# Performance work log

Hardware: AMD Instinct MI355X
Metric: run time of the kernel (lower is better)

The kernel has to match this reference:

```python
import jax, jax.numpy as jnp
import numpy as np
from jax import lax

H, P, N, G, K, CHUNK = 64, 64, 128, 1, 4, 256
D_MODEL = 2048
D_INNER = H * P            # 4096
CONV_DIM = D_INNER + 2 * G * N  # 4352
EPS = 1e-5


def setup_inputs() -> dict:
    key = jax.random.key(0)
    ks = jax.random.split(key, 6)
    s = lambda k, shape, scale: jax.random.normal(k, shape, jnp.float32) * scale
    return {
        "hidden_states": s(ks[0], (2, 2048, D_MODEL), 1.0),
        "in_proj_w": s(ks[1], (D_MODEL, D_INNER + CONV_DIM + H), D_MODEL ** -0.5),
        "conv_w": s(ks[2], (CONV_DIM, K), K ** -0.5),
        "conv_b": jnp.zeros((CONV_DIM,), jnp.float32),
        "dt_bias": jnp.ones((H,), jnp.float32),
        "A_log": jnp.log(jnp.arange(1, H + 1, dtype=jnp.float32)),
        "D_param": jnp.ones((H,), jnp.float32),
        "norm_w": jnp.ones((D_INNER,), jnp.float32),
        "out_proj_w": s(ks[3], (D_INNER, D_MODEL), D_INNER ** -0.5),
    }


def _mamba2_forward(hidden_states, in_proj_w, conv_w, conv_b, dt_bias, A_log, D_param, norm_w, out_proj_w):
    b, l, _ = hidden_states.shape
    c = l // CHUNK  # number of chunks

    # in_proj -> gate | conv channels (x,B,C) | dt
    proj = hidden_states @ in_proj_w
    gate = proj[..., :D_INNER]
    hbc = proj[..., D_INNER:D_INNER + CONV_DIM]
    dt = proj[..., D_INNER + CONV_DIM:]  # [b,l,H]

    # depthwise causal conv1d + silu
    xt = hbc.transpose(0, 2, 1)  # [b, CONV_DIM, l]
    y = lax.conv_general_dilated(
        xt, conv_w[:, None, :], window_strides=(1,), padding=[(K - 1, 0)],
        feature_group_count=CONV_DIM, dimension_numbers=("NCH", "OIH", "NCH"))
    hbc = jax.nn.silu(y + conv_b[None, :, None]).transpose(0, 2, 1)  # [b,l,CONV_DIM]

    # split into x / B / C per group (unflatten over groups as in torch code)
    per_g = D_INNER // G
    hg = hbc.reshape(b, l, G, per_g + 2 * N)
    x = hg[..., :per_g].reshape(b, l, H, P)                 # [b,l,h,p]
    Bm = hg[..., per_g:per_g + N]                            # [b,l,g,n]
    Cm = hg[..., per_g + N:]                                 # [b,l,g,n]
    hpg = H // G
    Bh = jnp.repeat(Bm, hpg, axis=2)                         # [b,l,h,n]
    Ch = jnp.repeat(Cm, hpg, axis=2)

    # dt: softplus(dt + bias), clamp per time_step_limit (0, inf)
    dt = jax.nn.softplus(dt + dt_bias)                       # [b,l,h]
    A = -jnp.exp(A_log)                                      # [h]

    # chunk the sequence
    x_c = x.reshape(b, c, CHUNK, H, P)
    B_c = Bh.reshape(b, c, CHUNK, H, N)
    C_c = Ch.reshape(b, c, CHUNK, H, N)
    dt_c = dt.reshape(b, c, CHUNK, H)

    dA = dt_c * A[None, None, None, :]                       # [b,c,L,h]
    cum = jnp.cumsum(dA, axis=2)                             # [b,c,L,h]

    # intra-chunk (diagonal block): decay[i,j] = exp(cum_i - cum_j), i>=j
    diff = cum[:, :, :, None, :] - cum[:, :, None, :, :]     # [b,c,i,j,h]
    i = jnp.arange(CHUNK)
    mask = i[:, None] >= i[None, :]
    decay = jnp.exp(jnp.where(mask[None, None, :, :, None], diff, -jnp.inf))
    scores = jnp.einsum("bcihn,bcjhn->bcijh", C_c, B_c) * decay * dt_c[:, :, None, :, :]
    Y_diag = jnp.einsum("bcijh,bcjhp->bcihp", scores, x_c)   # [b,c,L,h,p]

    # per-chunk final states
    decay_states = jnp.exp(cum[:, :, -1:, :] - cum)          # [b,c,L,h]
    states = jnp.einsum("bclh,bclhn,bclhp->bchpn", decay_states * dt_c, B_c, x_c)
    chunk_decay = jnp.exp(cum[:, :, -1, :])                  # [b,c,h]

    # inter-chunk recurrence over chunks
    def step(prev, inp):
        st, cd = inp  # [b,h,p,n], [b,h]
        new = cd[:, :, None, None] * prev + st
        return new, prev

    init = jnp.zeros((b, H, P, N), hidden_states.dtype)
    _, prev_states = lax.scan(step, init, (jnp.moveaxis(states, 1, 0), jnp.moveaxis(chunk_decay, 1, 0)))
    prev_states = jnp.moveaxis(prev_states, 0, 1)            # [b,c,h,p,n]

    state_decay_out = jnp.exp(cum)                           # [b,c,L,h]
    Y_off = jnp.einsum("bclhn,bchpn,bclh->bclhp", C_c, prev_states, state_decay_out)

    yh = (Y_diag + Y_off).reshape(b, l, H, P) + D_param[None, None, :, None] * x
    yr = yh.reshape(b, l, D_INNER)

    # gated RMSNorm
    hidden = yr * jax.nn.silu(gate)
    var = jnp.mean(hidden * hidden, axis=-1, keepdims=True)
    hidden = hidden * lax.rsqrt(var + EPS) * norm_w

    return hidden @ out_proj_w


def reference(hidden_states, in_proj_w, conv_w, conv_b, dt_bias, A_log, D_param, norm_w, out_proj_w):
    return _mamba2_forward(hidden_states, in_proj_w, conv_w, conv_b, dt_bias, A_log, D_param, norm_w, out_proj_w)
```

## Files before the change

### kernel.cpp

```cpp
#include <hip/hip_runtime.h>
#include <hip/hip_bf16.h>


typedef __attribute__((ext_vector_type(8))) _Float16 f16x8;
typedef __attribute__((ext_vector_type(4))) float f32x4;

#define GLD16(gp, lp) __builtin_amdgcn_global_load_lds( \
    (__attribute__((address_space(1))) void*)(gp),      \
    (__attribute__((address_space(3))) void*)(lp), 16, 0, 0)

__device__ __forceinline__ unsigned short f2h(float v) {
  _Float16 h = (_Float16)v;
  return *reinterpret_cast<unsigned short*>(&h);
}
__device__ __forceinline__ float h2f(unsigned short u) {
  _Float16 h = *reinterpret_cast<_Float16*>(&u);
  return (float)h;
}
__device__ __forceinline__ float siluf(float x) { return x / (1.f + expf(-x)); }

__global__ __launch_bounds__(256) void cast_f16(const float* __restrict__ s,
                                                _Float16* __restrict__ d) {
  long i = ((long)blockIdx.x * 256 + threadIdx.x) * 4;
  float4 v = *reinterpret_cast<const float4*>(s + i);
  ushort4 u;
  u.x = f2h(v.x); u.y = f2h(v.y); u.z = f2h(v.z); u.w = f2h(v.w);
  *reinterpret_cast<ushort4*>(d + i) = u;
}

__global__ __launch_bounds__(256) void transpose_win(const float* __restrict__ src,
                                                     _Float16* __restrict__ dst) {
  __shared__ float tile[32][33];
  int c0 = blockIdx.x * 32, r0 = blockIdx.y * 32;
  int tx = threadIdx.x, ty = threadIdx.y;
#pragma unroll
  for (int i = 0; i < 4; i++)
    tile[ty + i * 8][tx] = src[(long)(r0 + ty + i * 8) * 8512 + c0 + tx];
  __syncthreads();
#pragma unroll
  for (int i = 0; i < 4; i++) {
    int c = c0 + ty + i * 8, r = r0 + tx;
    dst[(long)c * 2048 + r] = (_Float16)tile[tx][ty + i * 8];
  }
}

__global__ __launch_bounds__(256) void transpose_wout(const float* __restrict__ src,
                                                      _Float16* __restrict__ dst,
                                                      int R, int C) {
  __shared__ float tile[32][33];
  int c0 = blockIdx.x * 32, r0 = blockIdx.y * 32;
  int tx = threadIdx.x, ty = threadIdx.y;
#pragma unroll
  for (int i = 0; i < 4; i++)
    tile[ty + i * 8][tx] = src[(long)(r0 + ty + i * 8) * C + c0 + tx];
  __syncthreads();
#pragma unroll
  for (int i = 0; i < 4; i++) {
    int c = c0 + ty + i * 8, r = r0 + tx;
    dst[(long)c * R + r] = (_Float16)tile[tx][ty + i * 8];
  }
}

__global__ __launch_bounds__(512, 2) void gemm_in8(const _Float16* __restrict__ A,
                                                   const _Float16* __restrict__ Bt,
                                                   _Float16* __restrict__ gate,
                                                   float* __restrict__ hbcf) {
  __shared__ __attribute__((aligned(128))) char ldsB[131072];
  const int tid = threadIdx.x;
  const int lane = tid & 63;
  const int wv = tid >> 6;
  const int wr = wv >> 2, wc = wv & 3;
  const int wg = blockIdx.x;
  const int swz = (wg & 7) * 66 + (wg >> 3);
  const int bx = swz % 33, by = swz / 33;

  const int srow = tid >> 3;
  const int scolg = (tid & 7) ^ (srow & 7);
  const _Float16* Ab = A + (long)by * 256 * 2048 + (long)srow * 2048 + scolg * 8;
  const _Float16* Bb = Bt + (long)bx * 256 * 2048 + (long)srow * 2048 + scolg * 8;
  const int ldst = tid << 4;

#define STAGE_A(tau, h) do {                                              \
    const _Float16* g_ = Ab + (long)(h) * 262144 + (tau) * 64;            \
    char* l_ = ldsB + ((((tau) & 1) << 2) + (h)) * 16384 + ldst;          \
    GLD16(g_, l_); GLD16(g_ + 131072, l_ + 8192); } while (0)
#define STAGE_B(tau, h) do {                                              \
    const _Float16* g_ = Bb + (long)(h) * 262144 + (tau) * 64;            \
    char* l_ = ldsB + ((((tau) & 1) << 2) + 2 + (h)) * 16384 + ldst;      \
    GLD16(g_, l_); GLD16(g_ + 131072, l_ + 8192); } while (0)

  const int fr = lane & 15;
  const int c16 = (lane >> 4) ^ (fr & 7);
  const int aOff = wr * 16384 + fr * 128 + c16 * 16;
  const int bOff = (2 + (wc >> 1)) * 16384 + ((wc & 1) * 64 + fr) * 128 + c16 * 16;
#define RD_A(b, mi, k32) (*(const f16x8*)(ldsB + ((aOff + (b) * 65536 + (mi) * 2048) ^ ((k32) * 64))))
#define RD_B(b, ni, k32) (*(const f16x8*)(ldsB + ((bOff + (b) * 65536 + (ni) * 2048) ^ ((k32) * 64))))

#define BAR() __builtin_amdgcn_s_barrier()
#define WLG0() asm volatile("s_waitcnt lgkmcnt(0)" ::: "memory")
#define WLG8() asm volatile("s_waitcnt lgkmcnt(8)" ::: "memory")
#define WVM4() asm volatile("s_waitcnt vmcnt(4)" ::: "memory")

  f32x4 acc[8][4];
#pragma unroll
  for (int mi = 0; mi < 8; ++mi)
#pragma unroll
    for (int ni = 0; ni < 4; ++ni) acc[mi][ni] = f32x4{0.f, 0.f, 0.f, 0.f};

  STAGE_A(0, 0); STAGE_A(0, 1); STAGE_B(0, 0); STAGE_B(0, 1);
  STAGE_B(1, 0); STAGE_B(1, 1);
  WVM4(); BAR();

#define MFMA_Q(MI0, MI1, x0, x1, x2, x3, PB)                                        \
  __builtin_amdgcn_s_setprio(1);                                                    \
  _Pragma("unroll") for (int ni = 0; ni < 4; ++ni) {                                \
    acc[MI0][ni] = __builtin_amdgcn_mfma_f32_16x16x32_f16(x0, PB[ni][0], acc[MI0][ni], 0, 0, 0); \
    acc[MI0][ni] = __builtin_amdgcn_mfma_f32_16x16x32_f16(x1, PB[ni][1], acc[MI0][ni], 0, 0, 0); \
    acc[MI1][ni] = __builtin_amdgcn_mfma_f32_16x16x32_f16(x2, PB[ni][0], acc[MI1][ni], 0, 0, 0); \
    acc[MI1][ni] = __builtin_amdgcn_mfma_f32_16x16x32_f16(x3, PB[ni][1], acc[MI1][ni], 0, 0, 0); \
  }                                                                                 \
  __builtin_amdgcn_s_setprio(0);

  for (int u = 0; u < 16; ++u) {
    const int t1 = 2 * u + 1;
    const int t2 = (2 * u + 2) & 31;
    const int t3 = (2 * u + 3) & 31;
    f16x8 PB0[4][2];
#pragma unroll
    for (int ni = 0; ni < 4; ++ni) { PB0[ni][0] = RD_B(0, ni, 0); PB0[ni][1] = RD_B(0, ni, 1); }
    {
      f16x8 x0 = RD_A(0, 0, 0), x1 = RD_A(0, 0, 1), x2 = RD_A(0, 1, 0), x3 = RD_A(0, 1, 1);
      STAGE_A(t1, 0); WLG8(); BAR(); WLG0();
      MFMA_Q(0, 1, x0, x1, x2, x3, PB0) BAR();
    }
    {
      f16x8 x0 = RD_A(0, 2, 0), x1 = RD_A(0, 2, 1), x2 = RD_A(0, 3, 0), x3 = RD_A(0, 3, 1);
      STAGE_A(t1, 1); BAR(); WLG0();
      MFMA_Q(2, 3, x0, x1, x2, x3, PB0) BAR();
    }
    {
      f16x8 x0 = RD_A(0, 4, 0), x1 = RD_A(0, 4, 1), x2 = RD_A(0, 5, 0), x3 = RD_A(0, 5, 1);
      STAGE_B(t2, 0); BAR(); WLG0();
      MFMA_Q(4, 5, x0, x1, x2, x3, PB0) BAR();
    }
    {
      f16x8 x0 = RD_A(0, 6, 0), x1 = RD_A(0, 6, 1), x2 = RD_A(0, 7, 0), x3 = RD_A(0, 7, 1);
      STAGE_B(t2, 1); BAR(); WLG0();
      MFMA_Q(6, 7, x0, x1, x2, x3, PB0) WVM4(); BAR();
    }
    f16x8 PB1[4][2];
#pragma unroll
    for (int ni = 0; ni < 4; ++ni) { PB1[ni][0] = RD_B(1, ni, 0); PB1[ni][1] = RD_B(1, ni, 1); }
    {
      f16x8 x0 = RD_A(1, 0, 0), x1 = RD_A(1, 0, 1), x2 = RD_A(1, 1, 0), x3 = RD_A(1, 1, 1);
      STAGE_A(t2, 0); WLG8(); BAR(); WLG0();
      MFMA_Q(0, 1, x0, x1, x2, x3, PB1) BAR();
    }
    {
      f16x8 x0 = RD_A(1, 2, 0), x1 = RD_A(1, 2, 1), x2 = RD_A(1, 3, 0), x3 = RD_A(1, 3, 1);
      STAGE_A(t2, 1); BAR(); WLG0();
      MFMA_Q(2, 3, x0, x1, x2, x3, PB1) BAR();
    }
    {
      f16x8 x0 = RD_A(1, 4, 0), x1 = RD_A(1, 4, 1), x2 = RD_A(1, 5, 0), x3 = RD_A(1, 5, 1);
      STAGE_B(t3, 0); BAR(); WLG0();
      MFMA_Q(4, 5, x0, x1, x2, x3, PB1) BAR();
    }
    {
      f16x8 x0 = RD_A(1, 6, 0), x1 = RD_A(1, 6, 1), x2 = RD_A(1, 7, 0), x3 = RD_A(1, 7, 1);
      STAGE_B(t3, 1); BAR(); WLG0();
      MFMA_Q(6, 7, x0, x1, x2, x3, PB1) WVM4(); BAR();
    }
  }
  const int m0 = by * 256 + wr * 128;
  const int n0 = bx * 256 + wc * 64;
  const int cl = lane & 15, rq = (lane >> 4) * 4;
  if (bx < 16) {
#pragma unroll
    for (int mi = 0; mi < 8; ++mi)
#pragma unroll
      for (int r = 0; r < 4; ++r) {
        long rowoff = (long)(m0 + mi * 16 + rq + r) * 4096 + n0 + cl;
#pragma unroll
        for (int ni = 0; ni < 4; ++ni) gate[rowoff + ni * 16] = (_Float16)acc[mi][ni][r];
      }
  } else {
#pragma unroll
    for (int mi = 0; mi < 8; ++mi)
#pragma unroll
      for (int r = 0; r < 4; ++r) {
        long rowoff = (long)(m0 + mi * 16 + rq + r) * 4352 + (n0 - 4096) + cl;
#pragma unroll
        for (int ni = 0; ni < 4; ++ni) hbcf[rowoff + ni * 16] = acc[mi][ni][r];
      }
  }
#undef STAGE_A
#undef STAGE_B
#undef RD_A
#undef RD_B
}

__global__ __launch_bounds__(512, 2) void gemm_out8(const _Float16* __restrict__ A,
                                                    const _Float16* __restrict__ Bt,
                                                    float* __restrict__ Cp) {
  __shared__ __attribute__((aligned(128))) char ldsB[131072];
  const int tid = threadIdx.x;
  const int lane = tid & 63;
  const int wv = tid >> 6;
  const int wr = wv >> 2, wc = wv & 3;
  const int wg = blockIdx.x;
  const int z = wg >> 7;
  const int r7 = wg & 127;
  const int sw = (r7 & 7) * 16 + (r7 >> 3);
  const int by = sw >> 3, bx = sw & 7;

  const int srow = tid >> 3;
  const int scolg = (tid & 7) ^ (srow & 7);
  const _Float16* Ab = A + (long)by * 256 * 4096 + (long)z * 2048 +
                       (long)srow * 4096 + scolg * 8;
  const _Float16* Bb = Bt + (long)bx * 256 * 4096 + (long)z * 2048 +
                       (long)srow * 4096 + scolg * 8;
  const int ldst = tid << 4;

#define STAGE_A(tau, h) do {                                              \
    const _Float16* g_ = Ab + (long)(h) * 524288 + (tau) * 64;            \
    char* l_ = ldsB + ((((tau) & 1) << 2) + (h)) * 16384 + ldst;          \
    GLD16(g_, l_); GLD16(g_ + 262144, l_ + 8192); } while (0)
#define STAGE_B(tau, h) do {                                              \
    const _Float16* g_ = Bb + (long)(h) * 524288 + (tau) * 64;            \
    char* l_ = ldsB + ((((tau) & 1) << 2) + 2 + (h)) * 16384 + ldst;      \
    GLD16(g_, l_); GLD16(g_ + 262144, l_ + 8192); } while (0)

  const int fr = lane & 15;
  const int c16 = (lane >> 4) ^ (fr & 7);
  const int aOff = wr * 16384 + fr * 128 + c16 * 16;
  const int bOff = (2 + (wc >> 1)) * 16384 + ((wc & 1) * 64 + fr) * 128 + c16 * 16;
#define RD_A(b, mi, k32) (*(const f16x8*)(ldsB + ((aOff + (b) * 65536 + (mi) * 2048) ^ ((k32) * 64))))
#define RD_B(b, ni, k32) (*(const f16x8*)(ldsB + ((bOff + (b) * 65536 + (ni) * 2048) ^ ((k32) * 64))))

  f32x4 acc[8][4];
#pragma unroll
  for (int mi = 0; mi < 8; ++mi)
#pragma unroll
    for (int ni = 0; ni < 4; ++ni) acc[mi][ni] = f32x4{0.f, 0.f, 0.f, 0.f};

  STAGE_A(0, 0); STAGE_A(0, 1); STAGE_B(0, 0); STAGE_B(0, 1);
  STAGE_B(1, 0); STAGE_B(1, 1);
  WVM4(); BAR();

  for (int u = 0; u < 16; ++u) {
    const int t1 = 2 * u + 1;
    const int t2 = (2 * u + 2) & 31;
    const int t3 = (2 * u + 3) & 31;
    f16x8 PB0[4][2];
#pragma unroll
    for (int ni = 0; ni < 4; ++ni) { PB0[ni][0] = RD_B(0, ni, 0); PB0[ni][1] = RD_B(0, ni, 1); }
    {
      f16x8 x0 = RD_A(0, 0, 0), x1 = RD_A(0, 0, 1), x2 = RD_A(0, 1, 0), x3 = RD_A(0, 1, 1);
      STAGE_A(t1, 0); WLG8(); BAR(); WLG0();
      MFMA_Q(0, 1, x0, x1, x2, x3, PB0) BAR();
    }
    {
      f16x8 x0 = RD_A(0, 2, 0), x1 = RD_A(0, 2, 1), x2 = RD_A(0, 3, 0), x3 = RD_A(0, 3, 1);
      STAGE_A(t1, 1); BAR(); WLG0();
      MFMA_Q(2, 3, x0, x1, x2, x3, PB0) BAR();
    }
    {
      f16x8 x0 = RD_A(0, 4, 0), x1 = RD_A(0, 4, 1), x2 = RD_A(0, 5, 0), x3 = RD_A(0, 5, 1);
      STAGE_B(t2, 0); BAR(); WLG0();
      MFMA_Q(4, 5, x0, x1, x2, x3, PB0) BAR();
    }
    {
      f16x8 x0 = RD_A(0, 6, 0), x1 = RD_A(0, 6, 1), x2 = RD_A(0, 7, 0), x3 = RD_A(0, 7, 1);
      STAGE_B(t2, 1); BAR(); WLG0();
      MFMA_Q(6, 7, x0, x1, x2, x3, PB0) WVM4(); BAR();
    }
    f16x8 PB1[4][2];
#pragma unroll
    for (int ni = 0; ni < 4; ++ni) { PB1[ni][0] = RD_B(1, ni, 0); PB1[ni][1] = RD_B(1, ni, 1); }
    {
      f16x8 x0 = RD_A(1, 0, 0), x1 = RD_A(1, 0, 1), x2 = RD_A(1, 1, 0), x3 = RD_A(1, 1, 1);
      STAGE_A(t2, 0); WLG8(); BAR(); WLG0();
      MFMA_Q(0, 1, x0, x1, x2, x3, PB1) BAR();
    }
    {
      f16x8 x0 = RD_A(1, 2, 0), x1 = RD_A(1, 2, 1), x2 = RD_A(1, 3, 0), x3 = RD_A(1, 3, 1);
      STAGE_A(t2, 1); BAR(); WLG0();
      MFMA_Q(2, 3, x0, x1, x2, x3, PB1) BAR();
    }
    {
      f16x8 x0 = RD_A(1, 4, 0), x1 = RD_A(1, 4, 1), x2 = RD_A(1, 5, 0), x3 = RD_A(1, 5, 1);
      STAGE_B(t3, 0); BAR(); WLG0();
      MFMA_Q(4, 5, x0, x1, x2, x3, PB1) BAR();
    }
    {
      f16x8 x0 = RD_A(1, 6, 0), x1 = RD_A(1, 6, 1), x2 = RD_A(1, 7, 0), x3 = RD_A(1, 7, 1);
      STAGE_B(t3, 1); BAR(); WLG0();
      MFMA_Q(6, 7, x0, x1, x2, x3, PB1) WVM4(); BAR();
    }
  }
  const int m0 = by * 256 + wr * 128;
  const int n0 = bx * 256 + wc * 64;
  const int cl = lane & 15, rq = (lane >> 4) * 4;
  float* Cb = Cp + (long)z * 8388608;
#pragma unroll
  for (int mi = 0; mi < 8; ++mi)
#pragma unroll
    for (int r = 0; r < 4; ++r) {
      long rowoff = (long)(m0 + mi * 16 + rq + r) * 2048 + n0 + cl;
#pragma unroll
      for (int ni = 0; ni < 4; ++ni) Cb[rowoff + ni * 16] = acc[mi][ni][r];
    }
#undef STAGE_A
#undef STAGE_B
#undef RD_A
#undef RD_B
#undef BAR
#undef WLG0
#undef WLG8
#undef WVM4
#undef MFMA_Q
}

__global__ __launch_bounds__(256) void add_out(const float* __restrict__ p,
                                               float* __restrict__ o) {
  long i = ((long)blockIdx.x * 256 + threadIdx.x) * 4;
  float4 a = *reinterpret_cast<const float4*>(p + i);
  float4 b = *reinterpret_cast<const float4*>(p + 8388608 + i);
  float4 r;
  r.x = a.x + b.x; r.y = a.y + b.y; r.z = a.z + b.z; r.w = a.w + b.w;
  *reinterpret_cast<float4*>(o + i) = r;
}

__global__ __launch_bounds__(256) void gemm_bt(const _Float16* __restrict__ A,
                                               const _Float16* __restrict__ Bt,
                                               float* __restrict__ Cf,
                                               int K, int ldc,
                                               long zsA, long zsB, long zsC) {
  __shared__ uint4 As4[512];
  __shared__ uint4 Bs4[512];
  _Float16* As = (_Float16*)As4;
  _Float16* Bs = (_Float16*)Bs4;
  const int tid = threadIdx.x;
  const int wv = tid >> 6;
  const int lane = tid & 63;
  const _Float16* Ab = A + (long)blockIdx.z * zsA + (long)blockIdx.y * 128 * K;
  const _Float16* Bb = Bt + (long)blockIdx.z * zsB + (long)blockIdx.x * 128 * K;
  const int c0 = wv * 128 + lane;
  const int c1 = c0 + 64;
  const long ra0 = (long)(c0 >> 2) * K + (c0 & 3) * 8;
  const long ra1 = (long)(c1 >> 2) * K + (c1 & 3) * 8;
  f32x4 acc[4][4];
#pragma unroll
  for (int mi = 0; mi < 4; mi++)
#pragma unroll
    for (int ni = 0; ni < 4; ni++) acc[mi][ni] = f32x4{0.f, 0.f, 0.f, 0.f};
  const int mrow = (wv & 1) * 64 + (lane & 15);
  const int nrow = (wv >> 1) * 64 + (lane & 15);
  const int koff = (lane >> 4) * 8;
  for (int k0 = 0; k0 < K; k0 += 32) {
    GLD16(Ab + ra0 + k0, (char*)As + c0 * 16);
    GLD16(Ab + ra1 + k0, (char*)As + c1 * 16);
    GLD16(Bb + ra0 + k0, (char*)Bs + c0 * 16);
    GLD16(Bb + ra1 + k0, (char*)Bs + c1 * 16);
    __syncthreads();
    f16x8 af[4], bfr[4];
#pragma unroll
    for (int mi = 0; mi < 4; mi++)
      af[mi] = *(const f16x8*)(As + (mrow + mi * 16) * 32 + koff);
#pragma unroll
    for (int ni = 0; ni < 4; ni++)
      bfr[ni] = *(const f16x8*)(Bs + (nrow + ni * 16) * 32 + koff);
#pragma unroll
    for (int mi = 0; mi < 4; mi++)
#pragma unroll
      for (int ni = 0; ni < 4; ni++)
        acc[mi][ni] = __builtin_amdgcn_mfma_f32_16x16x32_f16(af[mi], bfr[ni],
                                                             acc[mi][ni], 0, 0, 0);
    __syncthreads();
  }
  const int m0 = blockIdx.y * 128 + (wv & 1) * 64;
  const int n0 = blockIdx.x * 128 + (wv >> 1) * 64;
  const int cl = lane & 15, rq = (lane >> 4) * 4;
  const long zc = (long)blockIdx.z * zsC;
#pragma unroll
  for (int mi = 0; mi < 4; mi++)
#pragma unroll
    for (int r = 0; r < 4; r++) {
      long rowoff = zc + (long)(m0 + mi * 16 + rq + r) * ldc + n0 + cl;
#pragma unroll
      for (int ni = 0; ni < 4; ni++) Cf[rowoff + ni * 16] = acc[mi][ni][r];
    }
}

__global__ __launch_bounds__(256) void dtz_kernel(const float* __restrict__ hs,
                                                  const float* __restrict__ Win,
                                                  float* __restrict__ zf) {
  __shared__ float Xs[4][2048];
  int t0 = blockIdx.x * 4;
  int tid = threadIdx.x;
#pragma unroll
  for (int i = 0; i < 8; i++) {
    int e = tid * 4 + i * 1024;
    int tok = e >> 11, k = e & 2047;
    *reinterpret_cast<float4*>(&Xs[tok][k]) =
        *reinterpret_cast<const float4*>(&hs[(long)(t0 + tok) * 2048 + k]);
  }
  __syncthreads();
  int h = tid & 63, tg = tid >> 6;
  float a0 = 0.f, a1 = 0.f, a2 = 0.f, a3 = 0.f;
  const float* wcol = Win + 8448 + h;
  for (int k = 0; k < 2048; k += 4) {
    a0 = fmaf(Xs[tg][k + 0], wcol[(long)(k + 0) * 8512], a0);
    a1 = fmaf(Xs[tg][k + 1], wcol[(long)(k + 1) * 8512], a1);
    a2 = fmaf(Xs[tg][k + 2], wcol[(long)(k + 2) * 8512], a2);
    a3 = fmaf(Xs[tg][k + 3], wcol[(long)(k + 3) * 8512], a3);
  }
  zf[(long)(t0 + tg) * 64 + h] = (a0 + a1) + (a2 + a3);
}

__global__ __launch_bounds__(256) void conv_silu_kernel(const float* __restrict__ hbcf,
                                                        const float* __restrict__ convw,
                                                        const float* __restrict__ convb,
                                                        _Float16* __restrict__ x16,
                                                        _Float16* __restrict__ B16,
                                                        _Float16* __restrict__ C16) {
  int q = blockIdx.x * 256 + threadIdx.x;
  int t = blockIdx.y;
  int l = t & 2047;
  const float* col = hbcf + (long)t * 4352 + q;
  float4 wq = *reinterpret_cast<const float4*>(convw + q * 4);
  float a = convb[q];
  if (l >= 3) a += col[-3 * 4352] * wq.x;
  if (l >= 2) a += col[-2 * 4352] * wq.y;
  if (l >= 1) a += col[-1 * 4352] * wq.z;
  a += col[0] * wq.w;
  _Float16 o = (_Float16)siluf(a);
  if (q < 4096) x16[(long)t * 4096 + q] = o;
  else if (q < 4224) B16[(long)t * 128 + (q - 4096)] = o;
  else C16[(long)t * 128 + (q - 4224)] = o;
}

__global__ __launch_bounds__(256) void xtrans(const unsigned short* __restrict__ src,
                                              unsigned short* __restrict__ dst) {
  __shared__ unsigned short tile[64][66];
  int c0 = blockIdx.x * 64, r0 = blockIdx.y * 64;
  int tx = threadIdx.x & 15, ty = threadIdx.x >> 4;
#pragma unroll
  for (int i = 0; i < 4; i++) {
    int r = ty + i * 16;
    ushort4 v = *(const ushort4*)&src[(long)(r0 + r) * 4096 + c0 + 4 * tx];
    tile[r][4 * tx] = v.x; tile[r][4 * tx + 1] = v.y;
    tile[r][4 * tx + 2] = v.z; tile[r][4 * tx + 3] = v.w;
  }
  __syncthreads();
#pragma unroll
  for (int i = 0; i < 4; i++) {
    int c = ty + i * 16;
    ushort4 v;
    v.x = tile[4 * tx + 0][c]; v.y = tile[4 * tx + 1][c];
    v.z = tile[4 * tx + 2][c]; v.w = tile[4 * tx + 3][c];
    *(ushort4*)&dst[(long)(c0 + c) * 4096 + r0 + 4 * tx] = v;
  }
}

__global__ __launch_bounds__(256) void dt_cum_kernel(const float* __restrict__ zf,
                                                     const float* __restrict__ dtb,
                                                     const float* __restrict__ Alog,
                                                     float* __restrict__ dt_f,
                                                     float* __restrict__ cum_f,
                                                     float* __restrict__ cuml) {
  int bc = blockIdx.x;
  int h = threadIdx.x & 63, seg = threadIdx.x >> 6;
  int t0 = bc * 256;
  float Ah = -expf(Alog[h]);
  float bias = dtb[h];
  __shared__ float segsum[4][64];
  float s = 0.f;
  for (int j = 0; j < 64; j++) {
    int t = t0 + seg * 64 + j;
    float z = zf[(long)t * 64 + h] + bias;
    float v = (z > 20.f) ? z : log1pf(expf(z));
    dt_f[(long)t * 64 + h] = v;
    s += v * Ah;
  }
  segsum[seg][h] = s;
  __syncthreads();
  float run = 0.f;
  for (int k = 0; k < seg; k++) run += segsum[k][h];
  for (int j = 0; j < 64; j++) {
    int t = t0 + seg * 64 + j;
    run += dt_f[(long)t * 64 + h] * Ah;
    cum_f[(long)t * 64 + h] = run;
  }
  if (seg == 3) cuml[bc * 64 + h] = run;
}

__global__ __launch_bounds__(256) void states_mfma(const unsigned short* __restrict__ xT16,
                                                   const unsigned short* __restrict__ B16,
                                                   const float* __restrict__ dt_f,
                                                   const float* __restrict__ cum_f,
                                                   const float* __restrict__ cuml,
                                                   float* __restrict__ states) {
  int h = blockIdx.x, bc = blockIdx.y;
  int t0 = bc * 256, tid = threadIdx.x;
  __shared__ float w_s[256];
  __shared__ unsigned short Aw[64 * 40];
  __shared__ unsigned short BT[128 * 40];
  {
    int t = t0 + tid;
    w_s[tid] = expf(cuml[bc * 64 + h] - cum_f[(long)t * 64 + h]) * dt_f[(long)t * 64 + h];
  }
  __syncthreads();
  int wv = tid >> 6, lane = tid & 63;
  int mr = lane & 15, koff = (lane >> 4) * 8;
  f32x4 acc[4][2];
#pragma unroll
  for (int mi = 0; mi < 4; mi++)
#pragma unroll
    for (int nj = 0; nj < 2; nj++) acc[mi][nj] = f32x4{0.f, 0.f, 0.f, 0.f};
  for (int kt = 0; kt < 8; kt++) {
    {
      int p = tid >> 2, tq = tid & 3;
      const unsigned short* g = &xT16[((long)(h * 64 + p)) * 4096 + t0 + kt * 32 + tq * 8];
      ushort4 u0 = *(const ushort4*)g, u1 = *(const ushort4*)(g + 4);
      const float* wp = &w_s[kt * 32 + tq * 8];
      ushort4 o0, o1;
      o0.x = f2h(h2f(u0.x) * wp[0]); o0.y = f2h(h2f(u0.y) * wp[1]);
      o0.z = f2h(h2f(u0.z) * wp[2]); o0.w = f2h(h2f(u0.w) * wp[3]);
      o1.x = f2h(h2f(u1.x) * wp[4]); o1.y = f2h(h2f(u1.y) * wp[5]);
      o1.z = f2h(h2f(u1.z) * wp[6]); o1.w = f2h(h2f(u1.w) * wp[7]);
      *(ushort4*)&Aw[p * 40 + tq * 8] = o0;
      *(ushort4*)&Aw[p * 40 + tq * 8 + 4] = o1;
    }
    {
      int tl = tid >> 3, ng = tid & 7;
      const unsigned short* g = &B16[((long)(t0 + kt * 32 + tl)) * 128 + ng * 16];
#pragma unroll
      for (int j = 0; j < 16; j++) BT[(ng * 16 + j) * 40 + tl] = g[j];
    }
    __syncthreads();
    f16x8 af[4], bf[2];
#pragma unroll
    for (int mi = 0; mi < 4; mi++)
      af[mi] = *(const f16x8*)&Aw[(mi * 16 + mr) * 40 + koff];
#pragma unroll
    for (int nj = 0; nj < 2; nj++)
      bf[nj] = *(const f16x8*)&BT[((wv * 2 + nj) * 16 + mr) * 40 + koff];
#pragma unroll
    for (int mi = 0; mi < 4; mi++)
#pragma unroll
      for (int nj = 0; nj < 2; nj++)
        acc[mi][nj] = __builtin_amdgcn_mfma_f32_16x16x32_f16(af[mi], bf[nj],
                                                             acc[mi][nj], 0, 0, 0);
    __syncthreads();
  }
  int cl = lane & 15, rq = (lane >> 4) * 4;
  long base = ((long)(bc * 64 + h)) * 8192;
#pragma unroll
  for (int mi = 0; mi < 4; mi++)
#pragma unroll
    for (int r = 0; r < 4; r++) {
      int p = mi * 16 + rq + r;
#pragma unroll
      for (int nj = 0; nj < 2; nj++) {
        int n = (wv * 2 + nj) * 16 + cl;
        states[base + p * 128 + n] = acc[mi][nj][r];
      }
    }
}

__global__ __launch_bounds__(256) void recur_kernel(float* __restrict__ states,
                                                    const float* __restrict__ cuml) {
  int bh = blockIdx.x;
  int b = bh >> 6, h = bh & 63;
  int tid = threadIdx.x;
  float4 prev[8];
#pragma unroll
  for (int j = 0; j < 8; j++) prev[j] = make_float4(0.f, 0.f, 0.f, 0.f);
  for (int c = 0; c < 8; c++) {
    int bc = b * 8 + c;
    float cd = expf(cuml[bc * 64 + h]);
    long base = (long)(bc * 64 + h) * 8192;
#pragma unroll
    for (int j = 0; j < 8; j++) {
      long o = base + j * 1024 + tid * 4;
      float4 st = *reinterpret_cast<const float4*>(&states[o]);
      *reinterpret_cast<float4*>(&states[o]) = prev[j];
      prev[j].x = fmaf(cd, prev[j].x, st.x);
      prev[j].y = fmaf(cd, prev[j].y, st.y);
      prev[j].z = fmaf(cd, prev[j].z, st.z);
      prev[j].w = fmaf(cd, prev[j].w, st.w);
    }
  }
}

__global__ __launch_bounds__(256) void yfused(const unsigned short* __restrict__ xT16,
                                              const unsigned short* __restrict__ x16,
                                              const unsigned short* __restrict__ C16,
                                              const float* __restrict__ CBT,
                                              const float* __restrict__ states,
                                              const float* __restrict__ dt_f,
                                              const float* __restrict__ cum_f,
                                              const float* __restrict__ Dp,
                                              float* __restrict__ Ysum) {
  int h = blockIdx.x, bc = blockIdx.y;
  int t0 = bc * 256, tid = threadIdx.x;
  __shared__ unsigned short Sb[256 * 40];
  __shared__ unsigned short Xb[64 * 264];
  __shared__ float cum_s[256], dt_s[256];
  int i = tid;
  cum_s[i] = cum_f[(long)(t0 + i) * 64 + h];
  dt_s[i] = dt_f[(long)(t0 + i) * 64 + h];
  {
    int p = tid >> 2, tq = tid & 3;
    const unsigned short* g = &xT16[((long)(h * 64 + p)) * 4096 + t0 + tq * 64];
    unsigned short* l = &Xb[p * 264 + tq * 64];
#pragma unroll
    for (int c = 0; c < 8; c++)
      *(uint4*)(l + c * 8) = *(const uint4*)(g + c * 8);
  }
  __syncthreads();
  float cum_i = cum_s[i];
  const float* cbrow = CBT + (long)bc * 65536 + (long)i * 256;
  int wv = tid >> 6, lane = tid & 63;
  int mr = lane & 15, koff = (lane >> 4) * 8;
  f32x4 acc[4][4];
#pragma unroll
  for (int mi = 0; mi < 4; mi++)
#pragma unroll
    for (int ni = 0; ni < 4; ni++) acc[mi][ni] = f32x4{0.f, 0.f, 0.f, 0.f};
  for (int kt = 0; kt < 8; kt++) {
    int k0 = kt * 32;
#pragma unroll
    for (int c = 0; c < 8; c++) {
      float4 cb = *(const float4*)&cbrow[k0 + c * 4];
      ushort4 o;
      {
        int j = k0 + c * 4 + 0;
        float s = (j <= i) ? cb.x * expf(cum_i - cum_s[j]) * dt_s[j] : 0.f;
        o.x = f2h(s);
      }
      {
        int j = k0 + c * 4 + 1;
        float s = (j <= i) ? cb.y * expf(cum_i - cum_s[j]) * dt_s[j] : 0.f;
        o.y = f2h(s);
      }
      {
        int j = k0 + c * 4 + 2;
        float s = (j <= i) ? cb.z * expf(cum_i - cum_s[j]) * dt_s[j] : 0.f;
        o.z = f2h(s);
      }
      {
        int j = k0 + c * 4 + 3;
        float s = (j <= i) ? cb.w * expf(cum_i - cum_s[j]) * dt_s[j] : 0.f;
        o.w = f2h(s);
      }
      *(ushort4*)&Sb[i * 40 + c * 4] = o;
    }
    __syncthreads();
    if (kt <= 2 * wv + 1) {
      f16x8 af[4], bf[4];
#pragma unroll
      for (int mi = 0; mi < 4; mi++)
        af[mi] = *(const f16x8*)&Sb[(64 * wv + mi * 16 + mr) * 40 + koff];
#pragma unroll
      for (int ni = 0; ni < 4; ni++)
        bf[ni] = *(const f16x8*)&Xb[(ni * 16 + mr) * 264 + k0 + koff];
#pragma unroll
      for (int mi = 0; mi < 4; mi++)
#pragma unroll
        for (int ni = 0; ni < 4; ni++)
          acc[mi][ni] = __builtin_amdgcn_mfma_f32_16x16x32_f16(af[mi], bf[ni],
                                                               acc[mi][ni], 0, 0, 0);
    }
    __syncthreads();
  }
  {
    int p = tid >> 2, nq = tid & 3;
    const float* g = &states[((long)(bc * 64 + h)) * 8192 + p * 128 + nq * 32];
    unsigned short* l = &Xb[p * 136 + nq * 32];
#pragma unroll
    for (int c = 0; c < 8; c++) {
      float4 v = *(const float4*)(g + c * 4);
      ushort4 u;
      u.x = f2h(v.x); u.y = f2h(v.y); u.z = f2h(v.z); u.w = f2h(v.w);
      *(ushort4*)(l + c * 4) = u;
    }
  }
  float fac_i = expf(cum_i);
  for (int kn = 0; kn < 4; kn++) {
    {
      const unsigned short* g = &C16[((long)(t0 + i)) * 128 + kn * 32];
#pragma unroll
      for (int c = 0; c < 8; c++) {
        ushort4 u = *(const ushort4*)(g + c * 4);
        ushort4 o;
        o.x = f2h(h2f(u.x) * fac_i); o.y = f2h(h2f(u.y) * fac_i);
        o.z = f2h(h2f(u.z) * fac_i); o.w = f2h(h2f(u.w) * fac_i);
        *(ushort4*)&Sb[i * 40 + c * 4] = o;
      }
    }
    __syncthreads();
    f16x8 af[4], bf[4];
#pragma unroll
    for (int mi = 0; mi < 4; mi++)
      af[mi] = *(const f16x8*)&Sb[(64 * wv + mi * 16 + mr) * 40 + koff];
#pragma unroll
    for (int ni = 0; ni < 4; ni++)
      bf[ni] = *(const f16x8*)&Xb[(ni * 16 + mr) * 136 + kn * 32 + koff];
#pragma unroll
    for (int mi = 0; mi < 4; mi++)
#pragma unroll
      for (int ni = 0; ni < 4; ni++)
        acc[mi][ni] = __builtin_amdgcn_mfma_f32_16x16x32_f16(af[mi], bf[ni],
                                                             acc[mi][ni], 0, 0, 0);
    __syncthreads();
  }
  float Dh = Dp[h];
  int cl = lane & 15, rq = (lane >> 4) * 4;
#pragma unroll
  for (int mi = 0; mi < 4; mi++)
#pragma unroll
    for (int r = 0; r < 4; r++) {
      long row = t0 + 64 * wv + mi * 16 + rq + r;
      float* yr = &Ysum[row * 4096 + h * 64];
      const unsigned short* xr = &x16[row * 4096 + h * 64];
#pragma unroll
      for (int ni = 0; ni < 4; ni++) {
        int p = ni * 16 + cl;
        yr[p] = acc[mi][ni][r] + Dh * h2f(xr[p]);
      }
    }
}

__global__ __launch_bounds__(256) void norm_kernel(const float* __restrict__ Ysum,
                                                   const _Float16* __restrict__ gate,
                                                   const float* __restrict__ nw,
                                                   _Float16* __restrict__ hid) {
  int t = blockIdx.x;
  int tid = threadIdx.x;
  float hv[16];
  float ss = 0.f;
#pragma unroll
  for (int k = 0; k < 4; k++) {
    int d = tid * 4 + k * 1024;
    float4 y = *reinterpret_cast<const float4*>(&Ysum[(long)t * 4096 + d]);
    ushort4 gu = *reinterpret_cast<const ushort4*>(gate + (long)t * 4096 + d);
    float h0 = y.x * siluf(h2f(gu.x)), h1 = y.y * siluf(h2f(gu.y));
    float h2 = y.z * siluf(h2f(gu.z)), h3 = y.w * siluf(h2f(gu.w));
    hv[k * 4 + 0] = h0; hv[k * 4 + 1] = h1; hv[k * 4 + 2] = h2; hv[k * 4 + 3] = h3;
    ss += h0 * h0 + h1 * h1 + h2 * h2 + h3 * h3;
  }
#pragma unroll
  for (int o = 32; o > 0; o >>= 1) ss += __shfl_down(ss, o, 64);
  __shared__ float ws4[4];
  if ((tid & 63) == 0) ws4[tid >> 6] = ss;
  __syncthreads();
  float var = (ws4[0] + ws4[1] + ws4[2] + ws4[3]) * (1.f / 4096.f);
  float scale = rsqrtf(var + 1e-5f);
#pragma unroll
  for (int k = 0; k < 4; k++) {
    int d = tid * 4 + k * 1024;
    ushort4 u;
#pragma unroll
    for (int c = 0; c < 4; c++)
      ((unsigned short*)&u)[c] = f2h(hv[k * 4 + c] * scale * nw[d + c]);
    *reinterpret_cast<ushort4*>(hid + (long)t * 4096 + d) = u;
  }
}

extern "C" void kernel_launch(void* const* d_in, const int* in_sizes, int n_in,
                              void* d_out, int out_size, void* d_ws, size_t ws_size,
                              hipStream_t stream) {
  (void)in_sizes; (void)n_in; (void)out_size; (void)ws_size;
  const float* hs    = (const float*)d_in[0];
  const float* Win   = (const float*)d_in[1];
  const float* convw = (const float*)d_in[2];
  const float* convb = (const float*)d_in[3];
  const float* dtb   = (const float*)d_in[4];
  const float* Alog  = (const float*)d_in[5];
  const float* Dp    = (const float*)d_in[6];
  const float* nw    = (const float*)d_in[7];
  const float* Wout  = (const float*)d_in[8];
  float* out = (float*)d_out;

  char* base = (char*)d_ws;
  size_t off = 0;
  auto take = [&](size_t n) { char* r = base + off; off += (n + 255) & ~(size_t)255; return r; };
  float*    hbcf  = (float*)take(4096UL * 4352 * 4);
  _Float16* gateh = (_Float16*)take(4096UL * 4096 * 2);
  _Float16* Ah    = (_Float16*)take(4096UL * 2048 * 2);
  _Float16* WtH   = (_Float16*)take(8448UL * 2048 * 2);
  _Float16* xT16  = (_Float16*)take(4096UL * 4096 * 2);
  _Float16* B16   = (_Float16*)take(4096UL * 128 * 2);
  _Float16* C16   = (_Float16*)take(4096UL * 128 * 2);
  float*    zf    = (float*)take(4096UL * 64 * 4);
  float*    dt_f  = (float*)take(4096UL * 64 * 4);
  float*    cum_f = (float*)take(4096UL * 64 * 4);
  float*    cuml  = (float*)take(16UL * 64 * 4);
  float*    CBT   = (float*)take(16UL * 256 * 256 * 4);
  float*    states= (float*)take(1024UL * 8192 * 4);
  float*    Ysum  = hbcf;
  float*    oparts= hbcf;
  _Float16* WoutT = Ah;
  _Float16* x16   = WtH;
  _Float16* hid   = (_Float16*)states;

  dim3 tb(32, 8);
  cast_f16<<<8192, 256, 0, stream>>>(hs, Ah);
  transpose_win<<<dim3(264, 64), tb, 0, stream>>>(Win, WtH);
  dtz_kernel<<<1024, 256, 0, stream>>>(hs, Win, zf);
  gemm_in8<<<dim3(528), 512, 0, stream>>>(Ah, WtH, gateh, hbcf);
  transpose_wout<<<dim3(64, 128), tb, 0, stream>>>(Wout, WoutT, 4096, 2048);
  conv_silu_kernel<<<dim3(17, 4096), 256, 0, stream>>>(hbcf, convw, convb, x16, B16, C16);
  dt_cum_kernel<<<16, 256, 0, stream>>>(zf, dtb, Alog, dt_f, cum_f, cuml);
  xtrans<<<dim3(64, 64), 256, 0, stream>>>((const unsigned short*)x16, (unsigned short*)xT16);
  gemm_bt<<<dim3(2, 2, 16), 256, 0, stream>>>(C16, B16, CBT, 128, 256,
                                              32768, 32768, 65536);
  states_mfma<<<dim3(64, 16), 256, 0, stream>>>((const unsigned short*)xT16,
                                                (const unsigned short*)B16,
                                                dt_f, cum_f, cuml, states);
  recur_kernel<<<128, 256, 0, stream>>>(states, cuml);
  yfused<<<dim3(64, 16), 256, 0, stream>>>((const unsigned short*)xT16,
                                           (const unsigned short*)x16,
                                           (const unsigned short*)C16,
                                           CBT, states, dt_f, cum_f, Dp, Ysum);
  norm_kernel<<<4096, 256, 0, stream>>>(Ysum, gateh, nw, hid);
  gemm_out8<<<dim3(256), 512, 0, stream>>>(hid, WoutT, oparts);
  add_out<<<8192, 256, 0, stream>>>(oparts, out);
}
```

Measured before the change: 787.2 us.

## Split-K the last column tile of input GEMM to remove tail wave

Assigns the 512 full output tiles to the first wave and splits the leftover 33rd column tile into 8 K-slices computed by 128 extra blocks. Partial sums go to a scratch buffer aliased onto the states workspace and a new add_rem kernel reduces them into hbcf. This targets the underfilled tail wave of 16 blocks, at the cost of extra partial-sum traffic and an extra launch.

Result: no change. 777.3 us (-1.3%).

```diff
diff --git a/kernel.cpp b/kernel.cpp
--- a/kernel.cpp
+++ b/kernel.cpp
@@ -64,20 +64,28 @@
 __global__ __launch_bounds__(512, 2) void gemm_in8(const _Float16* __restrict__ A,
                                                    const _Float16* __restrict__ Bt,
                                                    _Float16* __restrict__ gate,
-                                                   float* __restrict__ hbcf) {
+                                                   float* __restrict__ hbcf,
+                                                   float* __restrict__ rparts) {
   __shared__ __attribute__((aligned(128))) char ldsB[131072];
   const int tid = threadIdx.x;
   const int lane = tid & 63;
   const int wv = tid >> 6;
   const int wr = wv >> 2, wc = wv & 3;
   const int wg = blockIdx.x;
-  const int swz = (wg & 7) * 66 + (wg >> 3);
-  const int bx = swz % 33, by = swz / 33;
+  const bool rem = wg >= 512;
+  int by, bxn, kbase, zz;
+  if (!rem) {
+    const int swz = (wg & 7) * 64 + (wg >> 3);
+    by = swz >> 5; bxn = swz & 31; kbase = 0; zz = 0;
+  } else {
+    const int idx = wg - 512;
+    by = idx & 15; zz = idx >> 4; bxn = 32; kbase = zz * 256;
+  }
 
   const int srow = tid >> 3;
   const int scolg = (tid & 7) ^ (srow & 7);
-  const _Float16* Ab = A + (long)by * 256 * 2048 + (long)srow * 2048 + scolg * 8;
-  const _Float16* Bb = Bt + (long)bx * 256 * 2048 + (long)srow * 2048 + scolg * 8;
+  const _Float16* Ab = A + (long)by * 524288 + (long)srow * 2048 + scolg * 8 + kbase;
+  const _Float16* Bb = Bt + (long)bxn * 524288 + (long)srow * 2048 + scolg * 8 + kbase;
   const int ldst = tid << 4;
 
 #define STAGE_A(tau, h) do {                                              \
@@ -121,83 +129,117 @@
   }                                                                                 \
   __builtin_amdgcn_s_setprio(0);
 
-  for (int u = 0; u < 16; ++u) {
-    const int t1 = 2 * u + 1;
-    const int t2 = (2 * u + 2) & 31;
-    const int t3 = (2 * u + 3) & 31;
-    f16x8 PB0[4][2];
-#pragma unroll
-    for (int ni = 0; ni < 4; ++ni) { PB0[ni][0] = RD_B(0, ni, 0); PB0[ni][1] = RD_B(0, ni, 1); }
-    {
-      f16x8 x0 = RD_A(0, 0, 0), x1 = RD_A(0, 0, 1), x2 = RD_A(0, 1, 0), x3 = RD_A(0, 1, 1);
-      STAGE_A(t1, 0); WLG8(); BAR(); WLG0();
-      MFMA_Q(0, 1, x0, x1, x2, x3, PB0) BAR();
-    }
-    {
-      f16x8 x0 = RD_A(0, 2, 0), x1 = RD_A(0, 2, 1), x2 = RD_A(0, 3, 0), x3 = RD_A(0, 3, 1);
-      STAGE_A(t1, 1); BAR(); WLG0();
-      MFMA_Q(2, 3, x0, x1, x2, x3, PB0) BAR();
-    }
-    {
-      f16x8 x0 = RD_A(0, 4, 0), x1 = RD_A(0, 4, 1), x2 = RD_A(0, 5, 0), x3 = RD_A(0, 5, 1);
-      STAGE_B(t2, 0); BAR(); WLG0();
-      MFMA_Q(4, 5, x0, x1, x2, x3, PB0) BAR();
-    }
-    {
-      f16x8 x0 = RD_A(0, 6, 0), x1 = RD_A(0, 6, 1), x2 = RD_A(0, 7, 0), x3 = RD_A(0, 7, 1);
-      STAGE_B(t2, 1); BAR(); WLG0();
-      MFMA_Q(6, 7, x0, x1, x2, x3, PB0) WVM4(); BAR();
-    }
-    f16x8 PB1[4][2];
-#pragma unroll
-    for (int ni = 0; ni < 4; ++ni) { PB1[ni][0] = RD_B(1, ni, 0); PB1[ni][1] = RD_B(1, ni, 1); }
-    {
-      f16x8 x0 = RD_A(1, 0, 0), x1 = RD_A(1, 0, 1), x2 = RD_A(1, 1, 0), x3 = RD_A(1, 1, 1);
-      STAGE_A(t2, 0); WLG8(); BAR(); WLG0();
-      MFMA_Q(0, 1, x0, x1, x2, x3, PB1) BAR();
-    }
-    {
-      f16x8 x0 = RD_A(1, 2, 0), x1 = RD_A(1, 2, 1), x2 = RD_A(1, 3, 0), x3 = RD_A(1, 3, 1);
-      STAGE_A(t2, 1); BAR(); WLG0();
-      MFMA_Q(2, 3, x0, x1, x2, x3, PB1) BAR();
-    }
-    {
-      f16x8 x0 = RD_A(1, 4, 0), x1 = RD_A(1, 4, 1), x2 = RD_A(1, 5, 0), x3 = RD_A(1, 5, 1);
-      STAGE_B(t3, 0); BAR(); WLG0();
-      MFMA_Q(4, 5, x0, x1, x2, x3, PB1) BAR();
-    }
-    {
-      f16x8 x0 = RD_A(1, 6, 0), x1 = RD_A(1, 6, 1), x2 = RD_A(1, 7, 0), x3 = RD_A(1, 7, 1);
-      STAGE_B(t3, 1); BAR(); WLG0();
-      MFMA_Q(6, 7, x0, x1, x2, x3, PB1) WVM4(); BAR();
-    }
-  }
+#define ITER8(u, msk) do {                                                          \
+    const int t1 = (2 * (u) + 1) & (msk);                                           \
+    const int t2 = (2 * (u) + 2) & (msk);                                           \
+    const int t3 = (2 * (u) + 3) & (msk);                                           \
+    f16x8 PB0[4][2];                                                                \
+    _Pragma("unroll") for (int ni = 0; ni < 4; ++ni) {                              \
+      PB0[ni][0] = RD_B(0, ni, 0); PB0[ni][1] = RD_B(0, ni, 1); }                   \
+    {                                                                               \
+      f16x8 x0 = RD_A(0, 0, 0), x1 = RD_A(0, 0, 1), x2 = RD_A(0, 1, 0), x3 = RD_A(0, 1, 1); \
+      STAGE_A(t1, 0); WLG8(); BAR(); WLG0();                                        \
+      MFMA_Q(0, 1, x0, x1, x2, x3, PB0) BAR();                                      \
+    }                                                                               \
+    {                                                                               \
+      f16x8 x0 = RD_A(0, 2, 0), x1 = RD_A(0, 2, 1), x2 = RD_A(0, 3, 0), x3 = RD_A(0, 3, 1); \
+      STAGE_A(t1, 1); BAR(); WLG0();                                                \
+      MFMA_Q(2, 3, x0, x1, x2, x3, PB0) BAR();                                      \
+    }                                                                               \
+    {                                                                               \
+      f16x8 x0 = RD_A(0, 4, 0), x1 = RD_A(0, 4, 1), x2 = RD_A(0, 5, 0), x3 = RD_A(0, 5, 1); \
+      STAGE_B(t2, 0); BAR(); WLG0();                                                \
+      MFMA_Q(4, 5, x0, x1, x2, x3, PB0) BAR();                                      \
+    }                                                                               \
+    {                                                                               \
+      f16x8 x0 = RD_A(0, 6, 0), x1 = RD_A(0, 6, 1), x2 = RD_A(0, 7, 0), x3 = RD_A(0, 7, 1); \
+      STAGE_B(t2, 1); BAR(); WLG0();                                                \
+      MFMA_Q(6, 7, x0, x1, x2, x3, PB0) WVM4(); BAR();                              \
+    }                                                                               \
+    f16x8 PB1[4][2];                                                                \
+    _Pragma("unroll") for (int ni = 0; ni < 4; ++ni) {                              \
+      PB1[ni][0] = RD_B(1, ni, 0); PB1[ni][1] = RD_B(1, ni, 1); }                   \
+    {                                                                               \
+      f16x8 x0 = RD_A(1, 0, 0), x1 = RD_A(1, 0, 1), x2 = RD_A(1, 1, 0), x3 = RD_A(1, 1, 1); \
+      STAGE_A(t2, 0); WLG8(); BAR(); WLG0();                                        \
+      MFMA_Q(0, 1, x0, x1, x2, x3, PB1) BAR();                                      \
+    }                                                                               \
+    {                                                                               \
+      f16x8 x0 = RD_A(1, 2, 0), x1 = RD_A(1, 2, 1), x2 = RD_A(1, 3, 0), x3 = RD_A(1, 3, 1); \
+      STAGE_A(t2, 1); BAR(); WLG0();                                                \
+      MFMA_Q(2, 3, x0, x1, x2, x3, PB1) BAR();                                      \
+    }                                                                               \
+    {                                                                               \
+      f16x8 x0 = RD_A(1, 4, 0), x1 = RD_A(1, 4, 1), x2 = RD_A(1, 5, 0), x3 = RD_A(1, 5, 1); \
+      STAGE_B(t3, 0); BAR(); WLG0();                                                \
+      MFMA_Q(4, 5, x0, x1, x2, x3, PB1) BAR();                                      \
+    }                                                                               \
+    {                                                                               \
+      f16x8 x0 = RD_A(1, 6, 0), x1 = RD_A(1, 6, 1), x2 = RD_A(1, 7, 0), x3 = RD_A(1, 7, 1); \
+      STAGE_B(t3, 1); BAR(); WLG0();                                                \
+      MFMA_Q(6, 7, x0, x1, x2, x3, PB1) WVM4(); BAR();                              \
+    }                                                                               \
+  } while (0)
+
+  if (!rem) {
+    for (int u = 0; u < 16; ++u) ITER8(u, 31);
+  } else {
+    for (int u = 0; u < 2; ++u) ITER8(u, 3);
+  }
+
   const int m0 = by * 256 + wr * 128;
-  const int n0 = bx * 256 + wc * 64;
   const int cl = lane & 15, rq = (lane >> 4) * 4;
-  if (bx < 16) {
+  if (!rem) {
+    const int n0 = bxn * 256 + wc * 64;
+    if (bxn < 16) {
+#pragma unroll
+      for (int mi = 0; mi < 8; ++mi)
+#pragma unroll
+        for (int r = 0; r < 4; ++r) {
+          long rowoff = (long)(m0 + mi * 16 + rq + r) * 4096 + n0 + cl;
+#pragma unroll
+          for (int ni = 0; ni < 4; ++ni) gate[rowoff + ni * 16] = (_Float16)acc[mi][ni][r];
+        }
+    } else {
+#pragma unroll
+      for (int mi = 0; mi < 8; ++mi)
+#pragma unroll
+        for (int r = 0; r < 4; ++r) {
+          long rowoff = (long)(m0 + mi * 16 + rq + r) * 4352 + (n0 - 4096) + cl;
+#pragma unroll
+          for (int ni = 0; ni < 4; ++ni) hbcf[rowoff + ni * 16] = acc[mi][ni][r];
+        }
+    }
+  } else {
+    float* rp = rparts + (long)zz * 1048576;
+    const int ncol = wc * 64;
 #pragma unroll
     for (int mi = 0; mi < 8; ++mi)
 #pragma unroll
       for (int r = 0; r < 4; ++r) {
-        long rowoff = (long)(m0 + mi * 16 + rq + r) * 4096 + n0 + cl;
-#pragma unroll
-        for (int ni = 0; ni < 4; ++ni) gate[rowoff + ni * 16] = (_Float16)acc[mi][ni][r];
-      }
-  } else {
-#pragma unroll
-    for (int mi = 0; mi < 8; ++mi)
-#pragma unroll
-      for (int r = 0; r < 4; ++r) {
-        long rowoff = (long)(m0 + mi * 16 + rq + r) * 4352 + (n0 - 4096) + cl;
-#pragma unroll
-        for (int ni = 0; ni < 4; ++ni) hbcf[rowoff + ni * 16] = acc[mi][ni][r];
+        long rowoff = (long)(m0 + mi * 16 + rq + r) * 256 + ncol + cl;
+#pragma unroll
+        for (int ni = 0; ni < 4; ++ni) rp[rowoff + ni * 16] = acc[mi][ni][r];
       }
   }
 #undef STAGE_A
 #undef STAGE_B
 #undef RD_A
 #undef RD_B
+#undef ITER8
+}
+
+__global__ __launch_bounds__(256) void add_rem(const float* __restrict__ rp,
+                                               float* __restrict__ hbcf) {
+  long e = ((long)blockIdx.x * 256 + threadIdx.x) * 4;
+  float4 s = *reinterpret_cast<const float4*>(rp + e);
+#pragma unroll
+  for (int z = 1; z < 8; ++z) {
+    float4 v = *reinterpret_cast<const float4*>(rp + (long)z * 1048576 + e);
+    s.x += v.x; s.y += v.y; s.z += v.z; s.w += v.w;
+  }
+  long row = e >> 8, col = e & 255;
+  *reinterpret_cast<float4*>(hbcf + row * 4352 + 4096 + col) = s;
 }
 
 __global__ __launch_bounds__(512, 2) void gemm_out8(const _Float16* __restrict__ A,
@@ -803,6 +845,7 @@
   float*    states= (float*)take(1024UL * 8192 * 4);
   float*    Ysum  = hbcf;
   float*    oparts= hbcf;
+  float*    rparts= states;
   _Float16* WoutT = Ah;
   _Float16* x16   = WtH;
   _Float16* hid   = (_Float16*)states;
@@ -811,7 +854,8 @@
   cast_f16<<<8192, 256, 0, stream>>>(hs, Ah);
   transpose_win<<<dim3(264, 64), tb, 0, stream>>>(Win, WtH);
   dtz_kernel<<<1024, 256, 0, stream>>>(hs, Win, zf);
-  gemm_in8<<<dim3(528), 512, 0, stream>>>(Ah, WtH, gateh, hbcf);
+  gemm_in8<<<dim3(640), 512, 0, stream>>>(Ah, WtH, gateh, hbcf, rparts);
+  add_rem<<<1024, 256, 0, stream>>>(rparts, hbcf);
   transpose_wout<<<dim3(64, 128), tb, 0, stream>>>(Wout, WoutT, 4096, 2048);
   conv_silu_kernel<<<dim3(17, 4096), 256, 0, stream>>>(hbcf, convw, convb, x16, B16, C16);
   dt_cum_kernel<<<16, 256, 0, stream>>>(zf, dtb, Alog, dt_f, cum_f, cuml);
```
